# Performance work log

Measured on AMD Instinct MI355X. Metric: run time of the kernel, lower is better.

The kernel has to match this reference:

```python
import jax, jax.numpy as jnp
import numpy as np

B = 4; N_LIG = 150; N_PROT = 550; N = 700
H = 128; HEADS = 4; KPH = 32; HPH = 32
L = 6; K = 48; EDGE_CH = 128; CUTOFF = 10.0
PROT_F = 27; NUM_CLASSES = 13
LOG2 = 0.6931471805599453
FLAT = N * H  # 89600, matches fc1 in_features


def ssp(x):
    # ShiftedSoftplus
    return jax.nn.softplus(x) - LOG2


def lin(x, w, b):
    # torch Linear convention: w is [out, in]
    return jnp.einsum('...i,oi->...o', x, w) + b


def setup_inputs() -> dict:
    key = jax.random.key(0)
    ki = iter(jax.random.split(key, 40))

    def nrm(shape, fan_in):
        return jax.random.normal(next(ki), shape, jnp.float32) / np.sqrt(fan_in).astype(np.float32)

    lig_pos = jax.random.normal(next(ki), (B, N_LIG, 3), jnp.float32) * 3.0
    lig_t = jax.random.randint(next(ki), (B, N_LIG, 1), 0, NUM_CLASSES).astype(jnp.float32)
    state = jnp.concatenate([lig_pos, lig_t], axis=-1)  # [B, N_LIG, 4]
    protein_pos_v = jnp.concatenate([
        jax.random.normal(next(ki), (B, N_PROT, 3), jnp.float32) * 3.0,
        jax.random.normal(next(ki), (B, N_PROT, PROT_F), jnp.float32)], axis=-1)  # [B, N_PROT, 30]

    inp = dict(state=state, protein_pos_v=protein_pos_v)
    inp['w_prot'] = nrm((H, PROT_F), PROT_F); inp['b_prot'] = jnp.zeros((H,), jnp.float32)
    inp['w_lig'] = nrm((H, NUM_CLASSES), NUM_CLASSES); inp['b_lig'] = jnp.zeros((H,), jnp.float32)
    # per-layer stacked encoder params (grouped 1x1 conv == per-head linear, no bias)
    inp['wq'] = nrm((L, HEADS, KPH, HPH), HPH)
    inp['wk'] = nrm((L, HEADS, KPH, HPH), HPH)
    inp['wv'] = nrm((L, HEADS, HPH, HPH), HPH)
    inp['wkn1_w'] = nrm((L, KPH, EDGE_CH), EDGE_CH); inp['wkn1_b'] = jnp.zeros((L, KPH), jnp.float32)
    inp['wkn2_w'] = nrm((L, KPH, KPH), KPH); inp['wkn2_b'] = jnp.zeros((L, KPH), jnp.float32)
    inp['wkl_w'] = nrm((L, KPH, KPH), KPH); inp['wkl_b'] = jnp.zeros((L, KPH), jnp.float32)
    inp['wvn1_w'] = nrm((L, HPH, EDGE_CH), EDGE_CH); inp['wvn1_b'] = jnp.zeros((L, HPH), jnp.float32)
    inp['wvn2_w'] = nrm((L, HPH, HPH), HPH); inp['wvn2_b'] = jnp.zeros((L, HPH), jnp.float32)
    inp['wvl_w'] = nrm((L, HPH, HPH), HPH); inp['wvl_b'] = jnp.zeros((L, HPH), jnp.float32)
    inp['cen_w'] = nrm((L, H, H), H); inp['cen_b'] = jnp.zeros((L, H), jnp.float32)
    inp['out_w'] = nrm((L, H, H), H); inp['out_b'] = jnp.zeros((L, H), jnp.float32)
    inp['ln_g'] = jnp.ones((L, H), jnp.float32); inp['ln_b'] = jnp.zeros((L, H), jnp.float32)
    inp['fc1_w'] = nrm((128, FLAT), FLAT); inp['fc1_b'] = jnp.zeros((128,), jnp.float32)
    inp['fc2_w'] = nrm((64, 128), 128); inp['fc2_b'] = jnp.zeros((64,), jnp.float32)
    inp['fc3_w'] = nrm((1, 64), 64); inp['fc3_b'] = jnp.zeros((1,), jnp.float32)
    return inp


def reference(state, protein_pos_v, w_prot, b_prot, w_lig, b_lig, wq, wk, wv,
              wkn1_w, wkn1_b, wkn2_w, wkn2_b, wkl_w, wkl_b,
              wvn1_w, wvn1_b, wvn2_w, wvn2_b, wvl_w, wvl_b,
              cen_w, cen_b, out_w, out_b, ln_g, ln_b,
              fc1_w, fc1_b, fc2_w, fc2_b, fc3_w, fc3_b):
    lig_pos = state[..., :3]
    lig_t = jax.lax.stop_gradient(state[..., 3]).astype(jnp.int32)
    lig_oh = jax.nn.one_hot(lig_t, NUM_CLASSES, dtype=jnp.float32)
    prot_pos = protein_pos_v[..., :3]
    prot_v = protein_pos_v[..., 3:]
    # compose_context: stable sort by batch -> protein atoms then ligand atoms per complex
    h = jnp.concatenate([lin(prot_v, w_prot, b_prot), lin(lig_oh, w_lig, b_lig)], axis=1)  # [B,N,H]
    pos = jnp.concatenate([prot_pos, lig_pos], axis=1)  # [B,N,3]
    # kNN graph (k nearest neighbors, no self loops), batched per complex
    d2 = jnp.sum((pos[:, :, None, :] - pos[:, None, :, :]) ** 2, axis=-1)  # [B,N,N]
    d2 = d2 + jnp.eye(N, dtype=d2.dtype) * 1e9
    _, nbr = jax.lax.top_k(-d2, K)  # [B,N,K]
    dist = jnp.sqrt(jnp.take_along_axis(d2, nbr, axis=2))  # [B,N,K]
    # Gaussian smearing of edge lengths
    offset = jnp.linspace(0.0, CUTOFF, EDGE_CH)
    coeff = -0.5 / (offset[1] - offset[0]) ** 2
    edge_attr = jnp.exp(coeff * (dist[..., None] - offset) ** 2)  # [B,N,K,E]
    gat = jax.vmap(lambda a, i: a[i])  # per-batch neighbor gather
    for l in range(L):
        xh = h.reshape(B, N, HEADS, HPH)
        q = jnp.einsum('bnhd,hkd->bnhk', xh, wq[l])
        kx = jnp.einsum('bnhd,hkd->bnhk', xh, wk[l])
        vx = jnp.einsum('bnhd,hkd->bnhk', xh, wv[l])
        w_k = lin(ssp(lin(edge_attr, wkn1_w[l], wkn1_b[l])), wkn2_w[l], wkn2_b[l])  # [B,N,K,KPH]
        keys_j = lin(w_k[:, :, :, None, :] * gat(kx, nbr), wkl_w[l], wkl_b[l])  # [B,N,K,heads,KPH]
        qk = jnp.einsum('bnhk,bnmhk->bnmh', q, keys_j)  # per-edge attention logits
        alpha = jax.nn.softmax(qk, axis=2)  # scatter_softmax over each node's K edges
        w_v = lin(ssp(lin(edge_attr, wvn1_w[l], wvn1_b[l])), wvn2_w[l], wvn2_b[l])  # [B,N,K,HPH]
        msg = lin(w_v[:, :, :, None, :] * gat(vx, nbr), wvl_w[l], wvl_b[l])  # [B,N,K,heads,HPH]
        aggr = jnp.einsum('bnmh,bnmhd->bnhd', alpha, msg).reshape(B, N, H)
        x = lin(h, cen_w[l], cen_b[l]) + aggr
        mu = jnp.mean(x, axis=-1, keepdims=True)
        var = jnp.var(x, axis=-1, keepdims=True)
        x = (x - mu) / jnp.sqrt(var + 1e-5) * ln_g[l] + ln_b[l]
        h = h + lin(ssp(x), out_w[l], out_b[l])  # residual per interaction block
    # decoup_batch + pad_tensor: constant 700 nodes/complex -> plain reshape
    x = h.reshape(B, FLAT)
    x = jax.nn.relu(lin(x, fc1_w, fc1_b))
    x = jax.nn.relu(lin(x, fc2_w, fc2_b))
    return lin(x, fc3_w, fc3_b)  # [B,1]
```

## Files before the change

kernel.cpp:

```cpp
#include <hip/hip_runtime.h>
#include <hip/hip_fp16.h>
#include <math.h>

constexpr int cB   = 4;
constexpr int cNL  = 150;
constexpr int cNP  = 550;
constexpr int cN   = 700;
constexpr int cH   = 128;
constexpr int cHeads = 4;
constexpr int cL   = 6;
constexpr int cK   = 48;
constexpr int cPF  = 27;
constexpr int cNC  = 13;
constexpr int cFLAT = cN * cH;
constexpr int cEdges = cB * cN * cK;

constexpr int   TABN = 4096;
#define TAB_DMAX 11.0f
#define TAB_HT   (TAB_DMAX / (float)(TABN - 1))
#define TAB_INV  ((float)(TABN - 1) / TAB_DMAX)

#define RBF_STEP (10.0f / 127.0f)
#define RBF_COEFF (-0.5f / (RBF_STEP * RBF_STEP))
#define LOG2F_C 0.69314718055994530942f

__device__ __forceinline__ float sspf(float x) {
    float ax = fabsf(x);
    return fmaxf(x, 0.0f) + __logf(1.0f + __expf(-ax)) - LOG2F_C;
}

__device__ __forceinline__ int mbcnt64(unsigned long long m) {
    return __builtin_amdgcn_mbcnt_hi((unsigned)(m >> 32),
           __builtin_amdgcn_mbcnt_lo((unsigned)m, 0));
}

__global__ void __launch_bounds__(256) k_init(
    const float* __restrict__ wq, const float* __restrict__ wk, const float* __restrict__ wv,
    const float* __restrict__ wkn1_w, const float* __restrict__ wvn1_w,
    const float* __restrict__ wkn2_w, const float* __restrict__ wvn2_w,
    const float* __restrict__ wvl_w,
    const float* __restrict__ cen_w, const float* __restrict__ out_w,
    float* __restrict__ wqT, float* __restrict__ wkT, float* __restrict__ wvT,
    float* __restrict__ w1Tk, float* __restrict__ w1Tv,
    float* __restrict__ w2Tk, float* __restrict__ w2Tv,
    float* __restrict__ wvlT,
    float* __restrict__ cenT, float* __restrict__ outT,
    const float* __restrict__ state, const float* __restrict__ ppv,
    const float* __restrict__ w_prot, const float* __restrict__ b_prot,
    const float* __restrict__ w_lig, const float* __restrict__ b_lig,
    float* __restrict__ h, float* __restrict__ pos)
{
    if (blockIdx.x < 1320) {
        int idx = blockIdx.x * 256 + threadIdx.x;
        if (idx < 3 * 24576) {
            int seg = idx / 24576, i = idx % 24576;
            const float* src = seg == 0 ? wq : (seg == 1 ? wk : wv);
            float* dst = seg == 0 ? wqT : (seg == 1 ? wkT : wvT);
            int l = i / 4096, r = i % 4096;
            int hh = r / 1024, r2 = r % 1024;
            int d = r2 / 32, k = r2 % 32;
            dst[i] = src[(((size_t)l * 4 + hh) * 32 + k) * 32 + d];
            return;
        }
        idx -= 3 * 24576;
        if (idx < 2 * 24576) {
            int seg = idx / 24576, i = idx % 24576;
            const float* src = seg == 0 ? wkn1_w : wvn1_w;
            float* dst = seg == 0 ? w1Tk : w1Tv;
            int l = i / 4096, r = i % 4096;
            int c = r / 32, o = r % 32;
            dst[i] = src[((size_t)l * 32 + o) * 128 + c];
            return;
        }
        idx -= 2 * 24576;
        if (idx < 3 * 6144) {
            int seg = idx / 6144, i = idx % 6144;
            const float* src = seg == 0 ? wkn2_w : (seg == 1 ? wvn2_w : wvl_w);
            float* dst = seg == 0 ? w2Tk : (seg == 1 ? w2Tv : wvlT);
            int l = i / 1024, r = i % 1024;
            int c = r / 32, o = r % 32;
            dst[i] = src[((size_t)l * 32 + o) * 32 + c];
            return;
        }
        idx -= 3 * 6144;
        int seg = idx / 98304, i = idx % 98304;
        const float* src = seg == 0 ? cen_w : out_w;
        float* dst = seg == 0 ? cenT : outT;
        int l = i / 16384, r = i % 16384;
        int ii = r / 128, o = r % 128;
        dst[i] = src[((size_t)l * 128 + o) * 128 + ii];
        return;
    }
    int rel = blockIdx.x - 1320;
    int node = rel * 2 + (threadIdx.x >> 7);
    int b = node / cN, n = node % cN;
    int o = threadIdx.x & 127;
    int lane = threadIdx.x & 63;
    float out;
    if (n < cNP) {
        const float* src = ppv + ((size_t)b * cNP + n) * 30;
        float v = (lane < 30) ? src[lane] : 0.f;
        float s = b_prot[o];
        #pragma unroll
        for (int f = 0; f < cPF; f++) s += w_prot[o * cPF + f] * __shfl(v, 3 + f);
        out = s;
        if (o < 3) pos[((size_t)b * cN + n) * 3 + o] = v;
    } else {
        int nl = n - cNP;
        const float* src = state + ((size_t)b * cNL + nl) * 4;
        float v = (lane < 4) ? src[lane] : 0.f;
        int t = (int)__shfl(v, 3);
        out = w_lig[o * cNC + t] + b_lig[o];
        if (o < 3) pos[((size_t)b * cN + n) * 3 + o] = v;
    }
    h[((size_t)b * cN + n) * cH + o] = out;
}

__global__ void __launch_bounds__(256) k_knn(
    const float* __restrict__ pos, int* __restrict__ nbr, float* __restrict__ dist,
    const float* __restrict__ w1Tk, const float* __restrict__ wkn1_b,
    const float* __restrict__ w2Tk, const float* __restrict__ wkn2_b,
    const float* __restrict__ w1Tv, const float* __restrict__ wvn1_b,
    const float* __restrict__ w2Tv, const float* __restrict__ wvn2_b,
    float* __restrict__ tab,
    const float* __restrict__ hbuf,
    const float* __restrict__ wqT, const float* __restrict__ wkT, const float* __restrict__ wvT,
    float* __restrict__ q0, __half* __restrict__ kx0, __half* __restrict__ vx0)
{
    int tid = threadIdx.x;
    if (blockIdx.x < cN) {
        int lane = tid & 63;
        int node = blockIdx.x * 4 + (tid >> 6);
        int b = node / cN, n = node % cN;
        const float* pb = pos + (size_t)b * cN * 3;
        float px = pb[n * 3 + 0], py = pb[n * 3 + 1], pz = pb[n * 3 + 2];
        float d2v[11];
        #pragma unroll
        for (int s = 0; s < 11; s++) {
            int j = lane + s * 64;
            float d2 = 1e30f;
            if (j < cN) {
                float dx = pb[j * 3 + 0] - px;
                float dy = pb[j * 3 + 1] - py;
                float dz = pb[j * 3 + 2] - pz;
                d2 = dx * dx + dy * dy + dz * dz;
                if (j == n) d2 = 1e9f;
            }
            d2v[s] = d2;
        }
        unsigned p = 0;
        for (int bit = 30; bit >= 0; --bit) {
            unsigned t = p | (1u << bit);
            int cnt = 0;
            #pragma unroll
            for (int s = 0; s < 11; s++)
                cnt += __popcll(__ballot(__float_as_uint(d2v[s]) < t));
            if (cnt <= 47) p = t;
        }
        int c_lt = 0;
        #pragma unroll
        for (int s = 0; s < 11; s++)
            c_lt += __popcll(__ballot(__float_as_uint(d2v[s]) < p));
        int base = 0, ebase = c_lt, need = 48 - c_lt;
        #pragma unroll
        for (int s = 0; s < 11; s++) {
            unsigned u = __float_as_uint(d2v[s]);
            unsigned long long blt = __ballot(u < p);
            unsigned long long beq = __ballot(u == p);
            int posn = -1;
            int bl = mbcnt64(blt);
            if (u < p) posn = base + bl;
            base += __popcll(blt);
            int r = mbcnt64(beq);
            int cs = __popcll(beq);
            int take = need < cs ? need : cs;
            if (u == p && r < take) posn = ebase + r;
            ebase += take; need -= take;
            if (posn >= 0) {
                nbr[(size_t)node * cK + posn] = s * 64 + lane;
                dist[(size_t)node * cK + posn] = sqrtf(d2v[s]);
            }
        }
        return;
    }
    if (blockIdx.x < cN + TABN / 4) {
        int rel = blockIdx.x - cN;
        int lane = tid & 63;
        int e = rel * 4 + (tid >> 6);
        int side = lane >> 5, o = lane & 31;
        float d = (float)e * TAB_HT;
        float z = d * (127.0f / 10.0f);
        int c0 = (int)floorf(z) - 7;
        c0 = c0 < 0 ? 0 : (c0 > 112 ? 112 : c0);
        int i = lane & 15;
        float tt = d - RBF_STEP * (float)(c0 + i);
        float eav = __expf(RBF_COEFF * tt * tt);
        const float* w1T = (side ? w1Tv : w1Tk);
        const float* b1  = (side ? wvn1_b : wkn1_b);
        const float* w2T = (side ? w2Tv : w2Tk);
        const float* b2  = (side ? wvn2_b : wkn2_b);
        int srcb = side * 32;
        for (int l = 0; l < cL; l++) {
            float s = b1[l * 32 + o];
            const float* w1p = w1T + (size_t)l * 4096;
            #pragma unroll
            for (int ii = 0; ii < 16; ii++)
                s += w1p[(c0 + ii) * 32 + o] * __shfl(eav, ii);
            float t1 = sspf(s);
            float s2 = b2[l * 32 + o];
            const float* w2p = w2T + (size_t)l * 1024;
            #pragma unroll
            for (int cc = 0; cc < 32; cc++)
                s2 += w2p[cc * 32 + o] * __shfl(t1, srcb + cc);
            tab[((size_t)(l * TABN + e) * 2 + side) * 32 + o] = s2;
        }
        return;
    }
    int bn = (blockIdx.x - cN - TABN / 4) * 2 + (tid >> 7);
    int o = tid & 127;
    int hh = o >> 5, kq = o & 31;
    float hval = hbuf[(size_t)bn * cH + o];
    size_t wo = ((size_t)0 * 4 + hh) * 1024;
    const float* bq = wqT + wo;
    const float* bk = wkT + wo;
    const float* bv = wvT + wo;
    int srcb = (hh & 1) * 32;
    float sq = 0.f, sk = 0.f, sv = 0.f;
    #pragma unroll
    for (int d = 0; d < 32; d++) {
        float x = __shfl(hval, srcb + d);
        sq += bq[d * 32 + kq] * x;
        sk += bk[d * 32 + kq] * x;
        sv += bv[d * 32 + kq] * x;
    }
    q0[(size_t)bn * cH + o] = sq;
    kx0[(size_t)bn * cH + o] = __float2half(sk);
    vx0[(size_t)bn * cH + o] = __float2half(sv);
}

__global__ void __launch_bounds__(256) k_attn(
    int l,
    const float* __restrict__ h_in, const float* __restrict__ qr,
    const __half* __restrict__ kxr, const __half* __restrict__ vxr,
    const int* __restrict__ nbr, const float* __restrict__ dist,
    const float* __restrict__ tab,
    const float* __restrict__ wkl_w,
    const float* __restrict__ wvlT, const float* __restrict__ wvl_b,
    const float* __restrict__ cenT, const float* __restrict__ cen_b,
    const float* __restrict__ outT, const float* __restrict__ out_b,
    const float* __restrict__ ln_g, const float* __restrict__ ln_b,
    float* __restrict__ h_out,
    float* __restrict__ qw, __half* __restrict__ kxw, __half* __restrict__ vxw,
    const float* __restrict__ wqT, const float* __restrict__ wkT, const float* __restrict__ wvT)
{
    int tid = threadIdx.x;
    int g = tid >> 7;
    int o = tid & 127;
    int bn = blockIdx.x * 2 + g;
    int b = bn / cN;
    int hh = o >> 5, c = o & 31;
    int srcb = (hh & 1) * 32;

    __shared__ float sh_h[2][cH];
    __shared__ float sh_qk[2][cK * cHeads];
    __shared__ float sh_t[2][cH];
    __shared__ int   sh_nb[2][cK];
    __shared__ int   sh_idx[2][cK];
    __shared__ float sh_frac[2][cK];
    __shared__ float red[2][4];

    sh_h[g][o] = h_in[(size_t)bn * cH + o];
    float qv = qr[(size_t)bn * cH + o];
    if (o < cK) {
        sh_nb[g][o] = nbr[(size_t)bn * cK + o];
        float d = dist[(size_t)bn * cK + o];
        float z = d * TAB_INV;
        int idx = (int)z;
        if (idx > TABN - 2) idx = TABN - 2;
        sh_idx[g][o] = idx;
        sh_frac[g][o] = fminf(z - (float)idx, 1.0f);
    }
    __syncthreads();

    const float* wklp = wkl_w + l * 1024;
    float qt = 0.f;
    #pragma unroll 8
    for (int k = 0; k < 32; k++) qt += __shfl(qv, srcb + k) * wklp[k * 32 + c];

    const __half* kxb = kxr + (size_t)b * cN * cH;
    const __half* vxb = vxr + (size_t)b * cN * cH;
    const float* tabl = tab + (size_t)l * TABN * 64;

    #pragma unroll 4
    for (int m = 0; m < cK; m += 2) {
        int j0 = sh_nb[g][m], j1 = sh_nb[g][m + 1];
        float k0 = __half2float(kxb[(size_t)j0 * cH + o]);
        float k1 = __half2float(kxb[(size_t)j1 * cH + o]);
        const float* t0 = tabl + (size_t)sh_idx[g][m] * 64 + c;
        const float* t1p = tabl + (size_t)sh_idx[g][m + 1] * 64 + c;
        float w0 = t0[0] + sh_frac[g][m] * (t0[64] - t0[0]);
        float w1 = t1p[0] + sh_frac[g][m + 1] * (t1p[64] - t1p[0]);
        float pa = qt * w0 * k0;
        float pb = qt * w1 * k1;
        float x = (c & 1) ? pb : pa;
        float y = (c & 1) ? pa : pb;
        x += __shfl_xor(y, 1);
        x += __shfl_xor(x, 2);
        x += __shfl_xor(x, 4);
        x += __shfl_xor(x, 8);
        x += __shfl_xor(x, 16);
        if (c < 2) sh_qk[g][(m + c) * cHeads + hh] = x;
    }
    __syncthreads();

    {
        float v1 = sh_qk[g][c * cHeads + hh];
        float v2 = (c < cK - 32) ? sh_qk[g][(32 + c) * cHeads + hh] : -1e30f;
        float mx = fmaxf(v1, v2);
        #pragma unroll
        for (int off = 16; off; off >>= 1) mx = fmaxf(mx, __shfl_xor(mx, off));
        float e1 = __expf(v1 - mx);
        float e2 = (c < cK - 32) ? __expf(v2 - mx) : 0.f;
        float s = e1 + e2;
        #pragma unroll
        for (int off = 16; off; off >>= 1) s += __shfl_xor(s, off);
        float inv = 1.0f / s;
        sh_qk[g][c * cHeads + hh] = e1 * inv;
        if (c < cK - 32) sh_qk[g][(32 + c) * cHeads + hh] = e2 * inv;
    }
    __syncthreads();

    float t = 0.f;
    #pragma unroll 4
    for (int m = 0; m < cK; m++) {
        int j = sh_nb[g][m];
        const float* tv = tabl + (size_t)sh_idx[g][m] * 64 + 32 + c;
        float wv_ = tv[0] + sh_frac[g][m] * (tv[64] - tv[0]);
        t += sh_qk[g][m * cHeads + hh] * (wv_ * __half2float(vxb[(size_t)j * cH + o]));
    }
    sh_t[g][o] = t;
    __syncthreads();

    const float* wvlTp = wvlT + l * 1024;
    float aggr = wvl_b[l * 32 + c];
    #pragma unroll 8
    for (int i = 0; i < 32; i++) aggr += wvlTp[i * 32 + c] * sh_t[g][hh * 32 + i];

    const float* cenTp = cenT + (size_t)l * cH * cH;
    float x0 = 0.f, x1 = 0.f;
    #pragma unroll 4
    for (int i = 0; i < cH; i += 2) {
        x0 += cenTp[i * cH + o] * sh_h[g][i];
        x1 += cenTp[(i + 1) * cH + o] * sh_h[g][i + 1];
    }
    float x = cen_b[l * cH + o] + aggr + x0 + x1;

    float s1 = x, s2 = x * x;
    #pragma unroll
    for (int off = 32; off; off >>= 1) {
        s1 += __shfl_xor(s1, off);
        s2 += __shfl_xor(s2, off);
    }
    int wid = (o >> 6);
    if ((o & 63) == 0) { red[g][wid * 2] = s1; red[g][wid * 2 + 1] = s2; }
    __syncthreads();
    float tot1 = red[g][0] + red[g][2], tot2 = red[g][1] + red[g][3];
    float mu = tot1 * (1.0f / 128.0f);
    float var = tot2 * (1.0f / 128.0f) - mu * mu;
    float xn = (x - mu) * rsqrtf(var + 1e-5f);
    xn = xn * ln_g[l * cH + o] + ln_b[l * cH + o];
    float sx = sspf(xn);
    sh_t[g][o] = sx;
    __syncthreads();

    const float* outTp = outT + (size_t)l * cH * cH;
    float o0 = 0.f, o1 = 0.f;
    #pragma unroll 4
    for (int i = 0; i < cH; i += 2) {
        o0 += outTp[i * cH + o] * sh_t[g][i];
        o1 += outTp[(i + 1) * cH + o] * sh_t[g][i + 1];
    }
    float hnew = sh_h[g][o] + out_b[l * cH + o] + o0 + o1;
    h_out[(size_t)bn * cH + o] = hnew;

    if (l < cL - 1) {
        size_t wo = ((size_t)(l + 1) * 4 + hh) * 1024;
        const float* bq = wqT + wo;
        const float* bk = wkT + wo;
        const float* bv = wvT + wo;
        float sq = 0.f, sk = 0.f, sv = 0.f;
        #pragma unroll
        for (int d = 0; d < 32; d++) {
            float xv = __shfl(hnew, srcb + d);
            sq += bq[d * 32 + c] * xv;
            sk += bk[d * 32 + c] * xv;
            sv += bv[d * 32 + c] * xv;
        }
        qw[(size_t)bn * cH + o] = sq;
        kxw[(size_t)bn * cH + o] = __float2half(sk);
        vxw[(size_t)bn * cH + o] = __float2half(sv);
    }
}

__global__ void __launch_bounds__(256) k_fc1p(const float* __restrict__ hbuf,
                                              const float* __restrict__ w,
                                              float* __restrict__ partial)
{
    int o = blockIdx.x >> 2, qp = blockIdx.x & 3;
    int tid = threadIdx.x;
    constexpr int CH = cFLAT / 4;
    const float4* wr = (const float4*)(w + (size_t)o * cFLAT + qp * CH);
    float a[4] = {0.f, 0.f, 0.f, 0.f};
    for (int i = tid; i < CH / 4; i += 256) {
        float4 wv = wr[i];
        #pragma unroll
        for (int bb = 0; bb < 4; bb++) {
            float4 hv = ((const float4*)(hbuf + (size_t)bb * cFLAT + qp * CH))[i];
            a[bb] += wv.x * hv.x + wv.y * hv.y + wv.z * hv.z + wv.w * hv.w;
        }
    }
    #pragma unroll
    for (int off = 32; off; off >>= 1) {
        #pragma unroll
        for (int bb = 0; bb < 4; bb++) a[bb] += __shfl_xor(a[bb], off);
    }
    __shared__ float red[4][4];
    if ((tid & 63) == 0) {
        #pragma unroll
        for (int bb = 0; bb < 4; bb++) red[tid >> 6][bb] = a[bb];
    }
    __syncthreads();
    if (tid < 4) {
        float s = red[0][tid] + red[1][tid] + red[2][tid] + red[3][tid];
        partial[((size_t)o * 4 + qp) * 4 + tid] = s;
    }
}

__global__ void __launch_bounds__(512) k_head2(const float* __restrict__ partial,
                                               const float* __restrict__ fc1_b,
                                               const float* __restrict__ fc2_w,
                                               const float* __restrict__ fc2_b,
                                               const float* __restrict__ fc3_w,
                                               const float* __restrict__ fc3_b,
                                               float* __restrict__ out)
{
    int tid = threadIdx.x;
    __shared__ float y1[4][128];
    __shared__ float y2[4][64];
    {
        int bb = tid >> 7, o = tid & 127;
        float s = fc1_b[o];
        #pragma unroll
        for (int qp = 0; qp < 4; qp++) s += partial[((size_t)o * 4 + qp) * 4 + bb];
        y1[bb][o] = fmaxf(s, 0.f);
    }
    __syncthreads();
    if (tid < 256) {
        int bb = tid >> 6, o = tid & 63;
        float s = fc2_b[o];
        #pragma unroll 8
        for (int i = 0; i < 128; i++) s += fc2_w[o * 128 + i] * y1[bb][i];
        y2[bb][o] = fmaxf(s, 0.f);
    }
    __syncthreads();
    if (tid < 4) {
        float s = fc3_b[0];
        #pragma unroll 8
        for (int i = 0; i < 64; i++) s += fc3_w[i] * y2[tid][i];
        out[tid] = s;
    }
}

extern "C" void kernel_launch(void* const* d_in, const int* in_sizes, int n_in,
                              void* d_out, int out_size, void* d_ws, size_t ws_size,
                              hipStream_t stream) {
    const float* state  = (const float*)d_in[0];
    const float* ppv    = (const float*)d_in[1];
    const float* w_prot = (const float*)d_in[2];
    const float* b_prot = (const float*)d_in[3];
    const float* w_lig  = (const float*)d_in[4];
    const float* b_lig  = (const float*)d_in[5];
    const float* wq     = (const float*)d_in[6];
    const float* wk     = (const float*)d_in[7];
    const float* wv     = (const float*)d_in[8];
    const float* wkn1_w = (const float*)d_in[9];
    const float* wkn1_b = (const float*)d_in[10];
    const float* wkn2_w = (const float*)d_in[11];
    const float* wkn2_b = (const float*)d_in[12];
    const float* wkl_w  = (const float*)d_in[13];
    const float* wvn1_w = (const float*)d_in[15];
    const float* wvn1_b = (const float*)d_in[16];
    const float* wvn2_w = (const float*)d_in[17];
    const float* wvn2_b = (const float*)d_in[18];
    const float* wvl_w  = (const float*)d_in[19];
    const float* wvl_b  = (const float*)d_in[20];
    const float* cen_w  = (const float*)d_in[21];
    const float* cen_b  = (const float*)d_in[22];
    const float* out_w  = (const float*)d_in[23];
    const float* out_b  = (const float*)d_in[24];
    const float* ln_g   = (const float*)d_in[25];
    const float* ln_b   = (const float*)d_in[26];
    const float* fc1_w  = (const float*)d_in[27];
    const float* fc1_b  = (const float*)d_in[28];
    const float* fc2_w  = (const float*)d_in[29];
    const float* fc2_b  = (const float*)d_in[30];
    const float* fc3_w  = (const float*)d_in[31];
    const float* fc3_b  = (const float*)d_in[32];

    float* ws = (float*)d_ws;
    size_t off = 0;
    float* pos   = ws + off; off += (size_t)cB * cN * 3;
    float* h_a   = ws + off; off += (size_t)cB * cN * cH;
    float* h_b   = ws + off; off += (size_t)cB * cN * cH;
    float* qA    = ws + off; off += (size_t)cB * cN * cH;
    float* qB    = ws + off; off += (size_t)cB * cN * cH;
    __half* kA   = (__half*)(ws + off); off += (size_t)cB * cN * cH / 2;
    __half* vA   = (__half*)(ws + off); off += (size_t)cB * cN * cH / 2;
    __half* kB   = (__half*)(ws + off); off += (size_t)cB * cN * cH / 2;
    __half* vB   = (__half*)(ws + off); off += (size_t)cB * cN * cH / 2;
    float* distb = ws + off; off += (size_t)cEdges;
    int*   nbrb  = (int*)(ws + off); off += (size_t)cEdges;
    float* tabb  = ws + off; off += (size_t)cL * TABN * 64;
    float* wqT   = ws + off; off += 24576;
    float* wkT   = ws + off; off += 24576;
    float* wvT   = ws + off; off += 24576;
    float* w1Tk  = ws + off; off += 24576;
    float* w1Tv  = ws + off; off += 24576;
    float* w2Tk  = ws + off; off += 6144;
    float* w2Tv  = ws + off; off += 6144;
    float* wvlT  = ws + off; off += 6144;
    float* cenT  = ws + off; off += 98304;
    float* outT  = ws + off; off += 98304;
    float* partial = ws + off; off += 2048;

    k_init<<<2720, 256, 0, stream>>>(wq, wk, wv, wkn1_w, wvn1_w, wkn2_w, wvn2_w,
                                     wvl_w, cen_w, out_w,
                                     wqT, wkT, wvT, w1Tk, w1Tv, w2Tk, w2Tv, wvlT, cenT, outT,
                                     state, ppv, w_prot, b_prot, w_lig, b_lig, h_a, pos);
    k_knn<<<cN + TABN / 4 + cB * cN / 2, 256, 0, stream>>>(
        pos, nbrb, distb,
        w1Tk, wkn1_b, w2Tk, wkn2_b, w1Tv, wvn1_b, w2Tv, wvn2_b, tabb,
        h_a, wqT, wkT, wvT, qA, kA, vA);

    float* hc = h_a;
    float* hn = h_b;
    for (int l = 0; l < cL; l++) {
        float* qr = (l & 1) ? qB : qA;
        __half* kr = (l & 1) ? kB : kA;
        __half* vr = (l & 1) ? vB : vA;
        float* qw2 = (l & 1) ? qA : qB;
        __half* kw2 = (l & 1) ? kA : kB;
        __half* vw2 = (l & 1) ? vA : vB;
        k_attn<<<cB * cN / 2, 256, 0, stream>>>(l, hc, qr, kr, vr, nbrb, distb, tabb,
            wkl_w, wvlT, wvl_b, cenT, cen_b, outT, out_b, ln_g, ln_b,
            hn, qw2, kw2, vw2, wqT, wkT, wvT);
        float* tmp = hc; hc = hn; hn = tmp;
    }

    k_fc1p<<<512, 256, 0, stream>>>(hc, fc1_w, partial);
    k_head2<<<1, 512, 0, stream>>>(partial, fc1_b, fc2_w, fc2_b, fc3_w, fc3_b, (float*)d_out);
}
```

Measured before the change: 308.1 us.

## Store interpolation table as paired value/next-value float2 and split lookups across half-waves

The distance-filter lookup table now stores each entry together with the next entry's value as a float2, so a single 8-byte load gives both interpolation endpoints. In the attention loops each half of a wavefront interpolates a different edge of the pair and the results are exchanged with a cross-half shuffle, which halves the table loads per lane. This doubles the table's memory footprint and adds shuffles and selects in exchange for fewer scattered gather loads. The last table entry's second slot is never written, but the index clamp keeps reads away from it.

```diff
diff --git a/kernel.cpp b/kernel.cpp
--- a/kernel.cpp
+++ b/kernel.cpp
@@ -122,7 +122,7 @@
     const float* __restrict__ w2Tk, const float* __restrict__ wkn2_b,
     const float* __restrict__ w1Tv, const float* __restrict__ wvn1_b,
     const float* __restrict__ w2Tv, const float* __restrict__ wvn2_b,
-    float* __restrict__ tab,
+    float* __restrict__ tabP,
     const float* __restrict__ hbuf,
     const float* __restrict__ wqT, const float* __restrict__ wkT, const float* __restrict__ wvT,
     float* __restrict__ q0, __half* __restrict__ kx0, __half* __restrict__ vx0)
@@ -212,7 +212,9 @@
             #pragma unroll
             for (int cc = 0; cc < 32; cc++)
                 s2 += w2p[cc * 32 + o] * __shfl(t1, srcb + cc);
-            tab[((size_t)(l * TABN + e) * 2 + side) * 32 + o] = s2;
+            tabP[((((size_t)l * TABN + e) * 2 + side) * 32 + o) * 2] = s2;
+            if (e > 0)
+                tabP[((((size_t)l * TABN + (e - 1)) * 2 + side) * 32 + o) * 2 + 1] = s2;
         }
         return;
     }
@@ -243,7 +245,7 @@
     const float* __restrict__ h_in, const float* __restrict__ qr,
     const __half* __restrict__ kxr, const __half* __restrict__ vxr,
     const int* __restrict__ nbr, const float* __restrict__ dist,
-    const float* __restrict__ tab,
+    const float* __restrict__ tabP,
     const float* __restrict__ wkl_w,
     const float* __restrict__ wvlT, const float* __restrict__ wvl_b,
     const float* __restrict__ cenT, const float* __restrict__ cen_b,
@@ -256,10 +258,12 @@
     int tid = threadIdx.x;
     int g = tid >> 7;
     int o = tid & 127;
+    int lane = tid & 63;
     int bn = blockIdx.x * 2 + g;
     int b = bn / cN;
     int hh = o >> 5, c = o & 31;
     int srcb = (hh & 1) * 32;
+    int hi = lane >> 5;
 
     __shared__ float sh_h[2][cH];
     __shared__ float sh_qk[2][cK * cHeads];
@@ -289,17 +293,19 @@
 
     const __half* kxb = kxr + (size_t)b * cN * cH;
     const __half* vxb = vxr + (size_t)b * cN * cH;
-    const float* tabl = tab + (size_t)l * TABN * 64;
+    const float2* tab2 = (const float2*)tabP + (size_t)l * TABN * 64;
 
     #pragma unroll 4
     for (int m = 0; m < cK; m += 2) {
         int j0 = sh_nb[g][m], j1 = sh_nb[g][m + 1];
         float k0 = __half2float(kxb[(size_t)j0 * cH + o]);
         float k1 = __half2float(kxb[(size_t)j1 * cH + o]);
-        const float* t0 = tabl + (size_t)sh_idx[g][m] * 64 + c;
-        const float* t1p = tabl + (size_t)sh_idx[g][m + 1] * 64 + c;
-        float w0 = t0[0] + sh_frac[g][m] * (t0[64] - t0[0]);
-        float w1 = t1p[0] + sh_frac[g][m + 1] * (t1p[64] - t1p[0]);
+        int mm = m + hi;
+        float2 tp = tab2[((size_t)sh_idx[g][mm] * 2 + 0) * 32 + c];
+        float wmine = tp.x + sh_frac[g][mm] * (tp.y - tp.x);
+        float wother = __shfl_xor(wmine, 32);
+        float w0 = hi ? wother : wmine;
+        float w1 = hi ? wmine : wother;
         float pa = qt * w0 * k0;
         float pb = qt * w1 * k1;
         float x = (c & 1) ? pb : pa;
@@ -330,15 +336,22 @@
     }
     __syncthreads();
 
-    float t = 0.f;
+    float t0 = 0.f, t1 = 0.f;
     #pragma unroll 4
-    for (int m = 0; m < cK; m++) {
-        int j = sh_nb[g][m];
-        const float* tv = tabl + (size_t)sh_idx[g][m] * 64 + 32 + c;
-        float wv_ = tv[0] + sh_frac[g][m] * (tv[64] - tv[0]);
-        t += sh_qk[g][m * cHeads + hh] * (wv_ * __half2float(vxb[(size_t)j * cH + o]));
-    }
-    sh_t[g][o] = t;
+    for (int m = 0; m < cK; m += 2) {
+        int j0 = sh_nb[g][m], j1 = sh_nb[g][m + 1];
+        float v0 = __half2float(vxb[(size_t)j0 * cH + o]);
+        float v1 = __half2float(vxb[(size_t)j1 * cH + o]);
+        int mm = m + hi;
+        float2 sp = tab2[((size_t)sh_idx[g][mm] * 2 + 1) * 32 + c];
+        float wmine = sp.x + sh_frac[g][mm] * (sp.y - sp.x);
+        float wother = __shfl_xor(wmine, 32);
+        float w0 = hi ? wother : wmine;
+        float w1 = hi ? wmine : wother;
+        t0 += sh_qk[g][m * cHeads + hh] * (w0 * v0);
+        t1 += sh_qk[g][(m + 1) * cHeads + hh] * (w1 * v1);
+    }
+    sh_t[g][o] = t0 + t1;
     __syncthreads();
 
     const float* wvlTp = wvlT + l * 1024;
@@ -520,7 +533,7 @@
     __half* vB   = (__half*)(ws + off); off += (size_t)cB * cN * cH / 2;
     float* distb = ws + off; off += (size_t)cEdges;
     int*   nbrb  = (int*)(ws + off); off += (size_t)cEdges;
-    float* tabb  = ws + off; off += (size_t)cL * TABN * 64;
+    float* tabb  = ws + off; off += (size_t)cL * TABN * 64 * 2;
     float* wqT   = ws + off; off += 24576;
     float* wkT   = ws + off; off += 24576;
     float* wvT   = ws + off; off += 24576;
```

Result: no change. 310.9 us (+0.9%).
